# Kernel tuning notes

Hardware: AMD Instinct MI355X
Metric: run time of the kernel (lower is better)

Reference implementation:

```python
import jax, jax.numpy as jnp
import numpy as np

WIN = (2, 4, 4)
SHIFT = (1, 2, 2)
NUM_HEADS = 8
LN_EPS = 1e-5


def _rel_pos_index(ws):
    wt, wh, ww = ws
    coords = np.stack(np.meshgrid(np.arange(wt), np.arange(wh), np.arange(ww), indexing='ij'))
    cf = coords.reshape(3, -1)                      # [3, N]
    rel = cf[:, :, None] - cf[:, None, :]           # [3, N, N]
    rel = rel.transpose(1, 2, 0).copy()             # [N, N, 3]
    rel[..., 0] += wt - 1
    rel[..., 1] += wh - 1
    rel[..., 2] += ww - 1
    rel[..., 0] *= (2 * wh - 1) * (2 * ww - 1)
    rel[..., 1] *= 2 * ww - 1
    return rel.sum(-1)                              # [N, N] int

REL_IDX = _rel_pos_index(WIN)


def _layer_norm(x, w, b):
    mu = jnp.mean(x, axis=-1, keepdims=True)
    var = jnp.mean(jnp.square(x - mu), axis=-1, keepdims=True)
    return (x - mu) * jax.lax.rsqrt(var + LN_EPS) * w + b


def setup_inputs() -> dict:
    key = jax.random.key(0)
    ks = jax.random.split(key, 8)
    C, Cm = 256, 1024
    inp = {
        'x': jax.random.normal(ks[0], (2, 16, 64, 64, C), jnp.float32),
        'norm1_w': jnp.ones((C,), jnp.float32),
        'norm1_b': jnp.zeros((C,), jnp.float32),
        'qkv_w': jax.random.normal(ks[1], (C, 3 * C), jnp.float32) * 0.02,
        'qkv_b': jnp.zeros((3 * C,), jnp.float32),
        'proj_w': jax.random.normal(ks[2], (C, C), jnp.float32) * 0.02,
        'proj_b': jnp.zeros((C,), jnp.float32),
        'rel_bias_table': jax.random.normal(ks[3], (147, NUM_HEADS), jnp.float32) * 0.02,
        'norm2_w': jnp.ones((C,), jnp.float32),
        'norm2_b': jnp.zeros((C,), jnp.float32),
        'mlp_w1': jax.random.normal(ks[4], (C, Cm), jnp.float32) * 0.02,
        'mlp_b1': jnp.zeros((Cm,), jnp.float32),
        'mlp_w2': jax.random.normal(ks[5], (Cm, C), jnp.float32) * 0.02,
        'mlp_b2': jnp.zeros((C,), jnp.float32),
    }
    return inp


def reference(x, norm1_w, norm1_b, qkv_w, qkv_b, proj_w, proj_b,
              rel_bias_table, norm2_w, norm2_b, mlp_w1, mlp_b1, mlp_w2, mlp_b2):
    B, T, H, W, C = x.shape
    wT, wH, wW = WIN
    nh = NUM_HEADS
    d = C // nh
    scale = d ** (-0.5)
    N = wT * wH * wW

    shortcut = x
    h = _layer_norm(x, norm1_w, norm1_b)
    # cyclic shift (no attention mask is applied in the original block)
    h = jnp.roll(h, shift=(-SHIFT[0], -SHIFT[1], -SHIFT[2]), axis=(1, 2, 3))
    # window partition -> [B*nW, N, C]
    h = h.reshape(B, T // wT, wT, H // wH, wH, W // wW, wW, C)
    h = h.transpose(0, 1, 3, 5, 2, 4, 6, 7).reshape(-1, N, C)
    B_ = h.shape[0]

    qkv = (h @ qkv_w + qkv_b).reshape(B_, N, 3, nh, d).transpose(2, 0, 3, 1, 4)
    q, k, v = qkv[0] * scale, qkv[1], qkv[2]          # [B_, nh, N, d]
    attn = jnp.einsum('bhnd,bhmd->bhnm', q, k)        # [B_, nh, N, N]
    bias = rel_bias_table[REL_IDX].transpose(2, 0, 1)  # [nh, N, N]
    attn = jax.nn.softmax(attn + bias[None], axis=-1)
    o = jnp.einsum('bhnm,bhmd->bhnd', attn, v)
    o = o.transpose(0, 2, 1, 3).reshape(B_, N, C)
    o = o @ proj_w + proj_b

    # window reverse -> [B, T, H, W, C]
    o = o.reshape(B, T // wT, H // wH, W // wW, wT, wH, wW, C)
    o = o.transpose(0, 1, 4, 2, 5, 3, 6, 7).reshape(B, T, H, W, C)
    o = jnp.roll(o, shift=SHIFT, axis=(1, 2, 3))

    x = shortcut + o
    m = _layer_norm(x, norm2_w, norm2_b)
    m = jax.nn.gelu(m @ mlp_w1 + mlp_b1, approximate=False) @ mlp_w2 + mlp_b2
    return x + m
```

## Files before the change

kernel.cpp:

```cpp
#include <hip/hip_runtime.h>
#include <hip/hip_bf16.h>
#include <cstdint>
#include <cstddef>

typedef __attribute__((ext_vector_type(8)))  short  s16x8;
typedef __attribute__((ext_vector_type(4)))  float  fp32x4;
typedef __attribute__((ext_vector_type(16))) float  fp32x16;
typedef __attribute__((ext_vector_type(4)))  unsigned short u16x4;

static __device__ __forceinline__ float bf2f(unsigned short u) {
    union { unsigned int i; float f; } v; v.i = ((unsigned int)u) << 16; return v.f;
}
static __device__ __forceinline__ unsigned short f2bf(float f) {
    __hip_bfloat16 h = __float2bfloat16(f);
    return __builtin_bit_cast(unsigned short, h);
}

static __device__ __forceinline__ fp32x16 mfma32(s16x8 a, s16x8 b, fp32x16 c) {
    return __builtin_amdgcn_mfma_f32_32x32x16_bf16(a, b, c, 0, 0, 0);
}
static __device__ __forceinline__ fp32x4 mfma16(s16x8 a, s16x8 b, fp32x4 c) {
    return __builtin_amdgcn_mfma_f32_16x16x32_bf16(a, b, c, 0, 0, 0);
}

static __device__ __forceinline__ float wave_sum(float v) {
#pragma unroll
    for (int off = 32; off > 0; off >>= 1) v += __shfl_xor(v, off, 64);
    return v;
}

static __device__ __forceinline__ float gelu_f(float u) {
    float t = u * (1.0f + 0.044715f * u * u) * 1.595769122f;
    return u * (1.0f / (1.0f + __expf(-t)));
}

#define NTOK   131072
#define CDIM   256

__global__ void prep_kernel(const float* __restrict__ qkv_w, const float* __restrict__ proj_w,
                            const float* __restrict__ w1,    const float* __restrict__ w2,
                            const float* __restrict__ rel,
                            unsigned short* __restrict__ qkvT, unsigned short* __restrict__ projT,
                            unsigned short* __restrict__ w1T,  unsigned short* __restrict__ w2T,
                            float* __restrict__ btab) {
    int id = blockIdx.x * 256 + threadIdx.x;
    if (id < 196608) {
        int n = id >> 8, k = id & 255;
        qkvT[id] = f2bf(qkv_w[k * 768 + n]);
    } else if (id < 262144) {
        int e = id - 196608; int n = e >> 8, k = e & 255;
        projT[e] = f2bf(proj_w[k * 256 + n]);
    } else if (id < 524288) {
        int e = id - 262144; int n = e >> 8, k = e & 255;
        w1T[e] = f2bf(w1[k * 1024 + n]);
    } else if (id < 786432) {
        int e = id - 524288; int n = e >> 10, k = e & 1023;
        w2T[e] = f2bf(w2[k * 256 + n]);
    } else {
        int e = id - 786432;
        int h = e >> 10, rem = e & 1023, n = rem >> 5, m = rem & 31;
        int tn = n >> 4, hn = (n >> 2) & 3, wn = n & 3;
        int tm = m >> 4, hm = (m >> 2) & 3, wm = m & 3;
        int ridx = (tn - tm + 1) * 49 + (hn - hm + 3) * 7 + (wn - wm + 3);
        btab[e] = rel[ridx * 8 + h];
    }
}

__global__ __launch_bounds__(256) void ln_kernel(const float* __restrict__ in,
                                                 const float* __restrict__ w,
                                                 const float* __restrict__ b,
                                                 unsigned short* __restrict__ out) {
    int tid = threadIdx.x, lane = tid & 63, wid = tid >> 6;
    long r = (long)blockIdx.x * 4 + wid;
    int n = (int)(r & 31); int win = (int)(r >> 5);
    int b_ = win >> 11, tw = (win >> 8) & 7, hw = (win >> 4) & 15, ww = win & 15;
    int ti = n >> 4, hi = (n >> 2) & 3, wi = n & 3;
    int t = tw * 2 + ti, hh = hw * 4 + hi, wv = ww * 4 + wi;
    int ts = (t + 1) & 15, hs = (hh + 2) & 63, wsd = (wv + 2) & 63;
    long src = ((long)((b_ * 16 + ts) * 64 + hs)) * 64 + wsd;

    float4 v = *(const float4*)&in[src * CDIM + lane * 4];
    float vv[4] = {v.x, v.y, v.z, v.w};
    float s = vv[0] + vv[1] + vv[2] + vv[3];
    s = wave_sum(s);
    float mean = s * (1.0f / 256.0f);
    float q = vv[0]*vv[0] + vv[1]*vv[1] + vv[2]*vv[2] + vv[3]*vv[3];
    q = wave_sum(q);
    float var = q * (1.0f / 256.0f) - mean * mean;
    float rstd = rsqrtf(var + 1e-5f);
    int c0 = lane * 4;
    u16x4 o;
#pragma unroll
    for (int j = 0; j < 4; ++j)
        o[j] = f2bf((vv[j] - mean) * rstd * w[c0 + j] + b[c0 + j]);
    *(u16x4*)&out[r * CDIM + c0] = o;
}

template <int K, int EPI, int NS, int NX>
__global__ __launch_bounds__(512) void gemm256(const unsigned short* __restrict__ A,
                                               const unsigned short* __restrict__ Bt,
                                               const float* __restrict__ bias,
                                               float* __restrict__ outf,
                                               unsigned short* __restrict__ outb,
                                               const float* __restrict__ resid,
                                               const float* __restrict__ lnw,
                                               const float* __restrict__ lnb) {
    extern __shared__ unsigned short lds[];
    const int tid = threadIdx.x;
    const int lane = tid & 63, wid = tid >> 6;
    const int wm = wid >> 2, wn = wid & 3;
    constexpr int NWG = NX * 512;
    constexpr int CPX = NWG / 8;
    const int bid = blockIdx.x;
    const int wg = (bid & 7) * CPX + (bid >> 3);
    const int n0 = (wg % NX) * 256;
    const size_t m0 = (size_t)(wg / NX) * 256;
    constexpr int NK = K / 64;

    fp32x4 acc[8][4] = {};

    auto stage = [&](int kt, int buf) {
#pragma unroll
        for (int i = 0; i < 4; ++i) {
            int L = i * 512 + tid;
            int r = L >> 3, c = L & 7;
            int sc = c ^ (r & 7);
            const unsigned short* ga = A + (m0 + r) * K + kt * 64 + sc * 8;
            __builtin_amdgcn_global_load_lds(
                (const __attribute__((address_space(1))) void*)ga,
                (__attribute__((address_space(3))) void*)(lds + buf * 16384 + L * 8),
                16, 0, 0);
            const unsigned short* gb = Bt + (size_t)(n0 + r) * K + kt * 64 + sc * 8;
            __builtin_amdgcn_global_load_lds(
                (const __attribute__((address_space(1))) void*)gb,
                (__attribute__((address_space(3))) void*)(lds + 32768 + buf * 16384 + L * 8),
                16, 0, 0);
        }
    };

    stage(0, 0);
    __syncthreads();
    for (int kt = 0; kt < NK; ++kt) {
        if (kt + 1 < NK) stage(kt + 1, (kt + 1) & 1);
        const unsigned short* As = lds + (kt & 1) * 16384;
        const unsigned short* Bs = lds + 32768 + (kt & 1) * 16384;
#pragma unroll
        for (int ks = 0; ks < 2; ++ks) {
            s16x8 a[8], b[4];
#pragma unroll
            for (int m = 0; m < 8; ++m) {
                int row = wm * 128 + m * 16 + (lane & 15);
                int j = ks * 4 + (lane >> 4);
                a[m] = *(const s16x8*)(As + row * 64 + ((j ^ (row & 7)) << 3));
            }
#pragma unroll
            for (int n = 0; n < 4; ++n) {
                int row = wn * 64 + n * 16 + (lane & 15);
                int j = ks * 4 + (lane >> 4);
                b[n] = *(const s16x8*)(Bs + row * 64 + ((j ^ (row & 7)) << 3));
            }
#pragma unroll
            for (int m = 0; m < 8; ++m)
#pragma unroll
                for (int n = 0; n < 4; ++n)
                    acc[m][n] = mfma16(a[m], b[n], acc[m][n]);
        }
        __syncthreads();
    }

    float bv[4];
#pragma unroll
    for (int n = 0; n < 4; ++n) bv[n] = bias[n0 + wn * 64 + n * 16 + (lane & 15)];

    if (EPI == 1) {
        float* part = (float*)lds;
        float lw[4], lb[4];
#pragma unroll
        for (int n = 0; n < 4; ++n) {
            int gc = wn * 64 + n * 16 + (lane & 15);
            lw[n] = lnw[gc]; lb[n] = lnb[gc];
        }
#pragma unroll
        for (int m = 0; m < 8; ++m) {
#pragma unroll
            for (int rg = 0; rg < 4; ++rg) {
                int row_t = wm * 128 + m * 16 + ((lane >> 4) << 2) + rg;
                size_t gr = m0 + row_t;
                int win = (int)(gr >> 5), n_ = (int)(gr & 31);
                int b_ = win >> 11, tw = (win >> 8) & 7, hw = (win >> 4) & 15, ww = win & 15;
                int ti = n_ >> 4, hi = (n_ >> 2) & 3, wi = n_ & 3;
                int t = tw * 2 + ti, hh = hw * 4 + hi, wv = ww * 4 + wi;
                int ts = (t + 1) & 15, hs = (hh + 2) & 63, wsd = (wv + 2) & 63;
                size_t dst = ((size_t)((b_ * 16 + ts) * 64 + hs)) * 64 + wsd;
                float s = 0.f, q = 0.f;
#pragma unroll
                for (int n = 0; n < 4; ++n) {
                    int gc = wn * 64 + n * 16 + (lane & 15);
                    float v = acc[m][n][rg] + bv[n] + resid[dst * CDIM + gc];
                    outf[dst * CDIM + gc] = v;
                    acc[m][n][rg] = v;
                    s += v; q += v * v;
                }
#pragma unroll
                for (int off = 1; off < 16; off <<= 1) {
                    s += __shfl_xor(s, off, 16);
                    q += __shfl_xor(q, off, 16);
                }
                if ((lane & 15) == 0) {
                    part[(row_t * 4 + wn) * 2]     = s;
                    part[(row_t * 4 + wn) * 2 + 1] = q;
                }
            }
        }
        __syncthreads();
#pragma unroll
        for (int m = 0; m < 8; ++m) {
#pragma unroll
            for (int rg = 0; rg < 4; ++rg) {
                int row_t = wm * 128 + m * 16 + ((lane >> 4) << 2) + rg;
                size_t gr = m0 + row_t;
                int win = (int)(gr >> 5), n_ = (int)(gr & 31);
                int b_ = win >> 11, tw = (win >> 8) & 7, hw = (win >> 4) & 15, ww = win & 15;
                int ti = n_ >> 4, hi = (n_ >> 2) & 3, wi = n_ & 3;
                int t = tw * 2 + ti, hh = hw * 4 + hi, wv = ww * 4 + wi;
                int ts = (t + 1) & 15, hs = (hh + 2) & 63, wsd = (wv + 2) & 63;
                size_t dst = ((size_t)((b_ * 16 + ts) * 64 + hs)) * 64 + wsd;
                float4 p0 = *(const float4*)&part[row_t * 8];
                float4 p1 = *(const float4*)&part[row_t * 8 + 4];
                float s = p0.x + p0.z + p1.x + p1.z;
                float q = p0.y + p0.w + p1.y + p1.w;
                float mean = s * (1.0f / 256.0f);
                float var  = q * (1.0f / 256.0f) - mean * mean;
                float rstd = rsqrtf(var + 1e-5f);
#pragma unroll
                for (int n = 0; n < 4; ++n) {
                    int gc = wn * 64 + n * 16 + (lane & 15);
                    float v = acc[m][n][rg];
                    outb[dst * CDIM + gc] = f2bf((v - mean) * rstd * lw[n] + lb[n]);
                }
            }
        }
    } else {
#pragma unroll
        for (int m = 0; m < 8; ++m) {
#pragma unroll
            for (int rg = 0; rg < 4; ++rg) {
                int row_t = wm * 128 + m * 16 + ((lane >> 4) << 2) + rg;
                size_t gr = m0 + row_t;
#pragma unroll
                for (int n = 0; n < 4; ++n) {
                    int gc = n0 + wn * 64 + n * 16 + (lane & 15);
                    float v = acc[m][n][rg] + bv[n];
                    if (EPI == 0) {
                        outb[gr * NS + gc] = f2bf(v);
                    } else if (EPI == 2) {
                        outb[gr * NS + gc] = f2bf(gelu_f(v));
                    } else {
                        outf[gr * NS + gc] += v;
                    }
                }
            }
        }
    }
}

__global__ __launch_bounds__(256) void attn_kernel(const unsigned short* __restrict__ qkv,
                                                   const float* __restrict__ btab,
                                                   unsigned short* __restrict__ obuf) {
    __shared__ unsigned short sP[4][1280];
    __shared__ unsigned short sVt[4][1280];
    int tid = threadIdx.x, lane = tid & 63, wid = tid >> 6;
    int task = blockIdx.x * 4 + wid;
    int win = task >> 3, hh = task & 7;
    const unsigned short* base = qkv + (size_t)win * 32 * 768 + hh * 32;
    int q = lane & 31, h = lane >> 5;

    s16x8 v0 = *(const s16x8*)(base + 512 + q * 768 + h * 16);
    s16x8 v1 = *(const s16x8*)(base + 512 + q * 768 + h * 16 + 8);
#pragma unroll
    for (int j = 0; j < 8; ++j) {
        sVt[wid][(h * 16 + j) * 40 + q]     = (unsigned short)v0[j];
        sVt[wid][(h * 16 + 8 + j) * 40 + q] = (unsigned short)v1[j];
    }

    s16x8 aq0 = *(const s16x8*)(base + q * 768 + h * 8);
    s16x8 aq1 = *(const s16x8*)(base + q * 768 + 16 + h * 8);
    s16x8 bk0 = *(const s16x8*)(base + 256 + q * 768 + h * 8);
    s16x8 bk1 = *(const s16x8*)(base + 256 + q * 768 + 16 + h * 8);
    fp32x16 S = {0.0f};
    S = mfma32(aq0, bk0, S);
    S = mfma32(aq1, bk1, S);

    const float scale = 0.17677669529663687f;
    float pr[16];
#pragma unroll
    for (int r = 0; r < 16; ++r) {
        int row = (r & 3) + 8 * (r >> 2) + 4 * h;
        float bvv = btab[(hh * 32 + row) * 32 + q];
        pr[r] = S[r] * scale + bvv;
    }
#pragma unroll
    for (int r = 0; r < 16; ++r) {
        float mx = pr[r];
#pragma unroll
        for (int off = 16; off > 0; off >>= 1) mx = fmaxf(mx, __shfl_xor(mx, off, 64));
        float e = __expf(pr[r] - mx);
        float sm = e;
#pragma unroll
        for (int off = 16; off > 0; off >>= 1) sm += __shfl_xor(sm, off, 64);
        pr[r] = e * __builtin_amdgcn_rcpf(sm);
    }
#pragma unroll
    for (int r = 0; r < 16; ++r) {
        int row = (r & 3) + 8 * (r >> 2) + 4 * h;
        sP[wid][row * 40 + q] = f2bf(pr[r]);
    }
    __syncthreads();

    s16x8 pa0 = *(const s16x8*)&sP[wid][q * 40 + h * 8];
    s16x8 pa1 = *(const s16x8*)&sP[wid][q * 40 + 16 + h * 8];
    s16x8 vb0 = *(const s16x8*)&sVt[wid][q * 40 + h * 8];
    s16x8 vb1 = *(const s16x8*)&sVt[wid][q * 40 + 16 + h * 8];
    fp32x16 O = {0.0f};
    O = mfma32(pa0, vb0, O);
    O = mfma32(pa1, vb1, O);
#pragma unroll
    for (int r = 0; r < 16; ++r) {
        int row = (r & 3) + 8 * (r >> 2) + 4 * h;
        obuf[((size_t)win * 32 + row) * 256 + hh * 32 + q] = f2bf(O[r]);
    }
}

extern "C" void kernel_launch(void* const* d_in, const int* in_sizes, int n_in,
                              void* d_out, int out_size, void* d_ws, size_t ws_size,
                              hipStream_t stream) {
    const float* x      = (const float*)d_in[0];
    const float* n1w    = (const float*)d_in[1];
    const float* n1b    = (const float*)d_in[2];
    const float* qkv_w  = (const float*)d_in[3];
    const float* qkv_b  = (const float*)d_in[4];
    const float* proj_w = (const float*)d_in[5];
    const float* proj_b = (const float*)d_in[6];
    const float* rel    = (const float*)d_in[7];
    const float* n2w    = (const float*)d_in[8];
    const float* n2b    = (const float*)d_in[9];
    const float* w1     = (const float*)d_in[10];
    const float* b1     = (const float*)d_in[11];
    const float* w2     = (const float*)d_in[12];
    const float* b2     = (const float*)d_in[13];
    float* out = (float*)d_out;

    char* ws = (char*)d_ws;
    unsigned short* hwin = (unsigned short*)ws;
    unsigned short* big  = (unsigned short*)(ws + 67108864);
    unsigned short* obuf = big + 100663296;
    char* wreg = ws + 67108864 + 268435456;
    unsigned short* qkvT  = (unsigned short*)(wreg);
    unsigned short* projT = (unsigned short*)(wreg + 393216);
    unsigned short* w1T   = (unsigned short*)(wreg + 524288);
    unsigned short* w2T   = (unsigned short*)(wreg + 1048576);
    float*          btab  = (float*)(wreg + 1572864);

    prep_kernel<<<3104, 256, 0, stream>>>(qkv_w, proj_w, w1, w2, rel, qkvT, projT, w1T, w2T, btab);

    ln_kernel<<<NTOK / 4, 256, 0, stream>>>(x, n1w, n1b, hwin);

    gemm256<256, 0, 768, 3><<<1536, 512, 131072, stream>>>(hwin, qkvT, qkv_b, nullptr, big,
                                                           nullptr, nullptr, nullptr);

    attn_kernel<<<8192, 256, 0, stream>>>(big, btab, obuf);

    gemm256<256, 1, 256, 1><<<512, 512, 131072, stream>>>(obuf, projT, proj_b, out, hwin,
                                                          x, n2w, n2b);

    gemm256<256, 2, 1024, 4><<<2048, 512, 131072, stream>>>(hwin, w1T, b1, nullptr, big,
                                                            nullptr, nullptr, nullptr);

    gemm256<1024, 3, 256, 1><<<512, 512, 131072, stream>>>(big, w2T, b2, out, nullptr,
                                                           nullptr, nullptr, nullptr);
}
```

Baseline: 653.1 us.

## Switch QKV and MLP GEMMs to 128x128 tiles with two blocks per CU

Adds a gemm128 kernel: 256-thread blocks computing 128x128 tiles with static 64KB LDS, two blocks per CU, precomputed incrementing global pointers, and a single barrier per k-step. It replaces the 256x256 tile GEMM for the QKV, MLP1 and MLP2 GEMMs. The projection GEMM with the fused residual+LayerNorm epilogue keeps its own 256-tile kernel, with its inner loop reordered into quadrants to shorten fragment register lifetimes. The aim is more occupancy and better tail balance, at the cost of lower per-tile data reuse and more global and LDS traffic per FLOP.

New measurement: 685.4 us. +4.9%, slower.

```diff
diff --git a/kernel.cpp b/kernel.cpp
--- a/kernel.cpp
+++ b/kernel.cpp
@@ -8,9 +8,6 @@
 typedef __attribute__((ext_vector_type(16))) float  fp32x16;
 typedef __attribute__((ext_vector_type(4)))  unsigned short u16x4;
 
-static __device__ __forceinline__ float bf2f(unsigned short u) {
-    union { unsigned int i; float f; } v; v.i = ((unsigned int)u) << 16; return v.f;
-}
 static __device__ __forceinline__ unsigned short f2bf(float f) {
     __hip_bfloat16 h = __float2bfloat16(f);
     return __builtin_bit_cast(unsigned short, h);
@@ -97,24 +94,120 @@
 }
 
 template <int K, int EPI, int NS, int NX>
-__global__ __launch_bounds__(512) void gemm256(const unsigned short* __restrict__ A,
-                                               const unsigned short* __restrict__ Bt,
-                                               const float* __restrict__ bias,
-                                               float* __restrict__ outf,
-                                               unsigned short* __restrict__ outb,
-                                               const float* __restrict__ resid,
-                                               const float* __restrict__ lnw,
-                                               const float* __restrict__ lnb) {
+__global__ __launch_bounds__(256, 2) void gemm128(const unsigned short* __restrict__ A,
+                                                  const unsigned short* __restrict__ Bt,
+                                                  const float* __restrict__ bias,
+                                                  float* __restrict__ outf,
+                                                  unsigned short* __restrict__ outb) {
+    __shared__ unsigned short lds[32768];
+    const int tid = threadIdx.x;
+    const int lane = tid & 63, wid = tid >> 6;
+    const int wm = wid >> 1, wn = wid & 1;
+    constexpr int NWG = 1024 * NX;
+    constexpr int CPX = NWG / 8;
+    const int bid = blockIdx.x;
+    const int wg = (bid & 7) * CPX + (bid >> 3);
+    const int n0 = (wg % NX) * 128;
+    const size_t m0 = (size_t)(wg / NX) * 128;
+    constexpr int NK = K / 64;
+
+    fp32x4 acc[4][4] = {};
+
+    const unsigned short* gA[4];
+    const unsigned short* gB[4];
+    int ldst[4];
+#pragma unroll
+    for (int i = 0; i < 4; ++i) {
+        int L = i * 256 + tid;
+        int r = L >> 3, c = L & 7;
+        int sc = c ^ (r & 7);
+        gA[i] = A  + (m0 + r) * (size_t)K + sc * 8;
+        gB[i] = Bt + (size_t)(n0 + r) * K + sc * 8;
+        ldst[i] = L * 8;
+    }
+    auto stage = [&](int buf) {
+#pragma unroll
+        for (int i = 0; i < 4; ++i) {
+            __builtin_amdgcn_global_load_lds(
+                (const __attribute__((address_space(1))) void*)gA[i],
+                (__attribute__((address_space(3))) void*)(lds + buf * 16384 + ldst[i]),
+                16, 0, 0);
+            __builtin_amdgcn_global_load_lds(
+                (const __attribute__((address_space(1))) void*)gB[i],
+                (__attribute__((address_space(3))) void*)(lds + buf * 16384 + 8192 + ldst[i]),
+                16, 0, 0);
+            gA[i] += 64; gB[i] += 64;
+        }
+    };
+
+    const int r7 = (lane & 15) & 7;
+    const int aoff = (wm * 64 + (lane & 15)) * 64 + (((lane >> 4) ^ r7) << 3);
+    const int boff = 8192 + (wn * 64 + (lane & 15)) * 64 + (((lane >> 4) ^ r7) << 3);
+
+    stage(0);
+    for (int kt = 0; kt < NK; ++kt) {
+        __syncthreads();
+        if (kt + 1 < NK) stage((kt + 1) & 1);
+        const int cb = (kt & 1) * 16384;
+#pragma unroll
+        for (int ks = 0; ks < 2; ++ks) {
+            const int kx = ks * 32;
+            s16x8 a[4], b[4];
+#pragma unroll
+            for (int m = 0; m < 4; ++m)
+                a[m] = *(const s16x8*)(lds + cb + (aoff ^ kx) + m * 1024);
+#pragma unroll
+            for (int n = 0; n < 4; ++n)
+                b[n] = *(const s16x8*)(lds + cb + (boff ^ kx) + n * 1024);
+#pragma unroll
+            for (int m = 0; m < 4; ++m)
+#pragma unroll
+                for (int n = 0; n < 4; ++n)
+                    acc[m][n] = mfma16(a[m], b[n], acc[m][n]);
+        }
+    }
+
+    float bv[4];
+#pragma unroll
+    for (int n = 0; n < 4; ++n) bv[n] = bias[n0 + wn * 64 + n * 16 + (lane & 15)];
+
+#pragma unroll
+    for (int m = 0; m < 4; ++m) {
+#pragma unroll
+        for (int rg = 0; rg < 4; ++rg) {
+            size_t gr = m0 + wm * 64 + m * 16 + ((lane >> 4) << 2) + rg;
+#pragma unroll
+            for (int n = 0; n < 4; ++n) {
+                int gc = n0 + wn * 64 + n * 16 + (lane & 15);
+                float v = acc[m][n][rg] + bv[n];
+                if (EPI == 0) {
+                    outb[gr * NS + gc] = f2bf(v);
+                } else if (EPI == 2) {
+                    outb[gr * NS + gc] = f2bf(gelu_f(v));
+                } else {
+                    outf[gr * NS + gc] += v;
+                }
+            }
+        }
+    }
+}
+
+template <int K>
+__global__ __launch_bounds__(512) void gemm256_proj(const unsigned short* __restrict__ A,
+                                                    const unsigned short* __restrict__ Bt,
+                                                    const float* __restrict__ bias,
+                                                    float* __restrict__ outf,
+                                                    unsigned short* __restrict__ outb,
+                                                    const float* __restrict__ resid,
+                                                    const float* __restrict__ lnw,
+                                                    const float* __restrict__ lnb) {
     extern __shared__ unsigned short lds[];
     const int tid = threadIdx.x;
     const int lane = tid & 63, wid = tid >> 6;
     const int wm = wid >> 2, wn = wid & 3;
-    constexpr int NWG = NX * 512;
-    constexpr int CPX = NWG / 8;
     const int bid = blockIdx.x;
-    const int wg = (bid & 7) * CPX + (bid >> 3);
-    const int n0 = (wg % NX) * 256;
-    const size_t m0 = (size_t)(wg / NX) * 256;
+    const int wg = (bid & 7) * 64 + (bid >> 3);
+    const size_t m0 = (size_t)wg * 256;
     constexpr int NK = K / 64;
 
     fp32x4 acc[8][4] = {};
@@ -130,7 +223,7 @@
                 (const __attribute__((address_space(1))) void*)ga,
                 (__attribute__((address_space(3))) void*)(lds + buf * 16384 + L * 8),
                 16, 0, 0);
-            const unsigned short* gb = Bt + (size_t)(n0 + r) * K + kt * 64 + sc * 8;
+            const unsigned short* gb = Bt + (size_t)r * K + kt * 64 + sc * 8;
             __builtin_amdgcn_global_load_lds(
                 (const __attribute__((address_space(1))) void*)gb,
                 (__attribute__((address_space(3))) void*)(lds + 32768 + buf * 16384 + L * 8),
@@ -139,126 +232,111 @@
     };
 
     stage(0, 0);
-    __syncthreads();
     for (int kt = 0; kt < NK; ++kt) {
+        __syncthreads();
         if (kt + 1 < NK) stage(kt + 1, (kt + 1) & 1);
         const unsigned short* As = lds + (kt & 1) * 16384;
         const unsigned short* Bs = lds + 32768 + (kt & 1) * 16384;
 #pragma unroll
-        for (int ks = 0; ks < 2; ++ks) {
-            s16x8 a[8], b[4];
-#pragma unroll
-            for (int m = 0; m < 8; ++m) {
-                int row = wm * 128 + m * 16 + (lane & 15);
-                int j = ks * 4 + (lane >> 4);
-                a[m] = *(const s16x8*)(As + row * 64 + ((j ^ (row & 7)) << 3));
+        for (int q = 0; q < 4; ++q) {
+            const int qm = q >> 1, qn = q & 1;
+            s16x8 a[4][2], b[2][2];
+#pragma unroll
+            for (int m = 0; m < 4; ++m)
+#pragma unroll
+                for (int ks = 0; ks < 2; ++ks) {
+                    int row = wm * 128 + qm * 64 + m * 16 + (lane & 15);
+                    int j = ks * 4 + (lane >> 4);
+                    a[m][ks] = *(const s16x8*)(As + row * 64 + ((j ^ (row & 7)) << 3));
+                }
+#pragma unroll
+            for (int n = 0; n < 2; ++n)
+#pragma unroll
+                for (int ks = 0; ks < 2; ++ks) {
+                    int row = wn * 64 + qn * 32 + n * 16 + (lane & 15);
+                    int j = ks * 4 + (lane >> 4);
+                    b[n][ks] = *(const s16x8*)(Bs + row * 64 + ((j ^ (row & 7)) << 3));
+                }
+#pragma unroll
+            for (int ks = 0; ks < 2; ++ks)
+#pragma unroll
+                for (int m = 0; m < 4; ++m)
+#pragma unroll
+                    for (int n = 0; n < 2; ++n)
+                        acc[qm * 4 + m][qn * 2 + n] =
+                            mfma16(a[m][ks], b[n][ks], acc[qm * 4 + m][qn * 2 + n]);
+        }
+        __syncthreads();
+    }
+
+    float bv[4];
+#pragma unroll
+    for (int n = 0; n < 4; ++n) bv[n] = bias[wn * 64 + n * 16 + (lane & 15)];
+
+    float* part = (float*)lds;
+    float lw[4], lb[4];
+#pragma unroll
+    for (int n = 0; n < 4; ++n) {
+        int gc = wn * 64 + n * 16 + (lane & 15);
+        lw[n] = lnw[gc]; lb[n] = lnb[gc];
+    }
+#pragma unroll
+    for (int m = 0; m < 8; ++m) {
+#pragma unroll
+        for (int rg = 0; rg < 4; ++rg) {
+            int row_t = wm * 128 + m * 16 + ((lane >> 4) << 2) + rg;
+            size_t gr = m0 + row_t;
+            int win = (int)(gr >> 5), n_ = (int)(gr & 31);
+            int b_ = win >> 11, tw = (win >> 8) & 7, hw = (win >> 4) & 15, ww = win & 15;
+            int ti = n_ >> 4, hi = (n_ >> 2) & 3, wi = n_ & 3;
+            int t = tw * 2 + ti, hh = hw * 4 + hi, wv = ww * 4 + wi;
+            int ts = (t + 1) & 15, hs = (hh + 2) & 63, wsd = (wv + 2) & 63;
+            size_t dst = ((size_t)((b_ * 16 + ts) * 64 + hs)) * 64 + wsd;
+            float s = 0.f, q = 0.f;
+#pragma unroll
+            for (int n = 0; n < 4; ++n) {
+                int gc = wn * 64 + n * 16 + (lane & 15);
+                float v = acc[m][n][rg] + bv[n] + resid[dst * CDIM + gc];
+                outf[dst * CDIM + gc] = v;
+                acc[m][n][rg] = v;
+                s += v; q += v * v;
             }
 #pragma unroll
+            for (int off = 1; off < 16; off <<= 1) {
+                s += __shfl_xor(s, off, 16);
+                q += __shfl_xor(q, off, 16);
+            }
+            if ((lane & 15) == 0) {
+                part[(row_t * 4 + wn) * 2]     = s;
+                part[(row_t * 4 + wn) * 2 + 1] = q;
+            }
+        }
+    }
+    __syncthreads();
+#pragma unroll
+    for (int m = 0; m < 8; ++m) {
+#pragma unroll
+        for (int rg = 0; rg < 4; ++rg) {
+            int row_t = wm * 128 + m * 16 + ((lane >> 4) << 2) + rg;
+            size_t gr = m0 + row_t;
+            int win = (int)(gr >> 5), n_ = (int)(gr & 31);
+            int b_ = win >> 11, tw = (win >> 8) & 7, hw = (win >> 4) & 15, ww = win & 15;
+            int ti = n_ >> 4, hi = (n_ >> 2) & 3, wi = n_ & 3;
+            int t = tw * 2 + ti, hh = hw * 4 + hi, wv = ww * 4 + wi;
+            int ts = (t + 1) & 15, hs = (hh + 2) & 63, wsd = (wv + 2) & 63;
+            size_t dst = ((size_t)((b_ * 16 + ts) * 64 + hs)) * 64 + wsd;
+            float4 p0 = *(const float4*)&part[row_t * 8];
+            float4 p1 = *(const float4*)&part[row_t * 8 + 4];
+            float s = p0.x + p0.z + p1.x + p1.z;
+            float q = p0.y + p0.w + p1.y + p1.w;
+            float mean = s * (1.0f / 256.0f);
+            float var  = q * (1.0f / 256.0f) - mean * mean;
+            float rstd = rsqrtf(var + 1e-5f);
+#pragma unroll
             for (int n = 0; n < 4; ++n) {
-                int row = wn * 64 + n * 16 + (lane & 15);
-                int j = ks * 4 + (lane >> 4);
-                b[n] = *(const s16x8*)(Bs + row * 64 + ((j ^ (row & 7)) << 3));
-            }
-#pragma unroll
-            for (int m = 0; m < 8; ++m)
-#pragma unroll
-                for (int n = 0; n < 4; ++n)
-                    acc[m][n] = mfma16(a[m], b[n], acc[m][n]);
-        }
-        __syncthreads();
-    }
-
-    float bv[4];
-#pragma unroll
-    for (int n = 0; n < 4; ++n) bv[n] = bias[n0 + wn * 64 + n * 16 + (lane & 15)];
-
-    if (EPI == 1) {
-        float* part = (float*)lds;
-        float lw[4], lb[4];
-#pragma unroll
-        for (int n = 0; n < 4; ++n) {
-            int gc = wn * 64 + n * 16 + (lane & 15);
-            lw[n] = lnw[gc]; lb[n] = lnb[gc];
-        }
-#pragma unroll
-        for (int m = 0; m < 8; ++m) {
-#pragma unroll
-            for (int rg = 0; rg < 4; ++rg) {
-                int row_t = wm * 128 + m * 16 + ((lane >> 4) << 2) + rg;
-                size_t gr = m0 + row_t;
-                int win = (int)(gr >> 5), n_ = (int)(gr & 31);
-                int b_ = win >> 11, tw = (win >> 8) & 7, hw = (win >> 4) & 15, ww = win & 15;
-                int ti = n_ >> 4, hi = (n_ >> 2) & 3, wi = n_ & 3;
-                int t = tw * 2 + ti, hh = hw * 4 + hi, wv = ww * 4 + wi;
-                int ts = (t + 1) & 15, hs = (hh + 2) & 63, wsd = (wv + 2) & 63;
-                size_t dst = ((size_t)((b_ * 16 + ts) * 64 + hs)) * 64 + wsd;
-                float s = 0.f, q = 0.f;
-#pragma unroll
-                for (int n = 0; n < 4; ++n) {
-                    int gc = wn * 64 + n * 16 + (lane & 15);
-                    float v = acc[m][n][rg] + bv[n] + resid[dst * CDIM + gc];
-                    outf[dst * CDIM + gc] = v;
-                    acc[m][n][rg] = v;
-                    s += v; q += v * v;
-                }
-#pragma unroll
-                for (int off = 1; off < 16; off <<= 1) {
-                    s += __shfl_xor(s, off, 16);
-                    q += __shfl_xor(q, off, 16);
-                }
-                if ((lane & 15) == 0) {
-                    part[(row_t * 4 + wn) * 2]     = s;
-                    part[(row_t * 4 + wn) * 2 + 1] = q;
-                }
-            }
-        }
-        __syncthreads();
-#pragma unroll
-        for (int m = 0; m < 8; ++m) {
-#pragma unroll
-            for (int rg = 0; rg < 4; ++rg) {
-                int row_t = wm * 128 + m * 16 + ((lane >> 4) << 2) + rg;
-                size_t gr = m0 + row_t;
-                int win = (int)(gr >> 5), n_ = (int)(gr & 31);
-                int b_ = win >> 11, tw = (win >> 8) & 7, hw = (win >> 4) & 15, ww = win & 15;
-                int ti = n_ >> 4, hi = (n_ >> 2) & 3, wi = n_ & 3;
-                int t = tw * 2 + ti, hh = hw * 4 + hi, wv = ww * 4 + wi;
-                int ts = (t + 1) & 15, hs = (hh + 2) & 63, wsd = (wv + 2) & 63;
-                size_t dst = ((size_t)((b_ * 16 + ts) * 64 + hs)) * 64 + wsd;
-                float4 p0 = *(const float4*)&part[row_t * 8];
-                float4 p1 = *(const float4*)&part[row_t * 8 + 4];
-                float s = p0.x + p0.z + p1.x + p1.z;
-                float q = p0.y + p0.w + p1.y + p1.w;
-                float mean = s * (1.0f / 256.0f);
-                float var  = q * (1.0f / 256.0f) - mean * mean;
-                float rstd = rsqrtf(var + 1e-5f);
-#pragma unroll
-                for (int n = 0; n < 4; ++n) {
-                    int gc = wn * 64 + n * 16 + (lane & 15);
-                    float v = acc[m][n][rg];
-                    outb[dst * CDIM + gc] = f2bf((v - mean) * rstd * lw[n] + lb[n]);
-                }
-            }
-        }
-    } else {
-#pragma unroll
-        for (int m = 0; m < 8; ++m) {
-#pragma unroll
-            for (int rg = 0; rg < 4; ++rg) {
-                int row_t = wm * 128 + m * 16 + ((lane >> 4) << 2) + rg;
-                size_t gr = m0 + row_t;
-#pragma unroll
-                for (int n = 0; n < 4; ++n) {
-                    int gc = n0 + wn * 64 + n * 16 + (lane & 15);
-                    float v = acc[m][n][rg] + bv[n];
-                    if (EPI == 0) {
-                        outb[gr * NS + gc] = f2bf(v);
-                    } else if (EPI == 2) {
-                        outb[gr * NS + gc] = f2bf(gelu_f(v));
-                    } else {
-                        outf[gr * NS + gc] += v;
-                    }
-                }
+                int gc = wn * 64 + n * 16 + (lane & 15);
+                float v = acc[m][n][rg];
+                outb[dst * CDIM + gc] = f2bf((v - mean) * rstd * lw[n] + lb[n]);
             }
         }
     }
@@ -296,8 +374,7 @@
 #pragma unroll
     for (int r = 0; r < 16; ++r) {
         int row = (r & 3) + 8 * (r >> 2) + 4 * h;
-        float bvv = btab[(hh * 32 + row) * 32 + q];
-        pr[r] = S[r] * scale + bvv;
+        pr[r] = S[r] * scale + btab[(hh * 32 + row) * 32 + q];
     }
 #pragma unroll
     for (int r = 0; r < 16; ++r) {
@@ -365,17 +442,13 @@
 
     ln_kernel<<<NTOK / 4, 256, 0, stream>>>(x, n1w, n1b, hwin);
 
-    gemm256<256, 0, 768, 3><<<1536, 512, 131072, stream>>>(hwin, qkvT, qkv_b, nullptr, big,
-                                                           nullptr, nullptr, nullptr);
+    gemm128<256, 0, 768, 6><<<6144, 256, 0, stream>>>(hwin, qkvT, qkv_b, nullptr, big);
 
     attn_kernel<<<8192, 256, 0, stream>>>(big, btab, obuf);
 
-    gemm256<256, 1, 256, 1><<<512, 512, 131072, stream>>>(obuf, projT, proj_b, out, hwin,
-                                                          x, n2w, n2b);
-
-    gemm256<256, 2, 1024, 4><<<2048, 512, 131072, stream>>>(hwin, w1T, b1, nullptr, big,
-                                                            nullptr, nullptr, nullptr);
-
-    gemm256<1024, 3, 256, 1><<<512, 512, 131072, stream>>>(big, w2T, b2, out, nullptr,
-                                                           nullptr, nullptr, nullptr);
-}
+    gemm256_proj<256><<<512, 512, 131072, stream>>>(obuf, projT, proj_b, out, hwin, x, n2w, n2b);
+
+    gemm128<256, 2, 1024, 8><<<8192, 256, 0, stream>>>(hwin, w1T, b1, nullptr, big);
+
+    gemm128<1024, 3, 256, 2><<<2048, 256, 0, stream>>>(big, w2T, b2, out, nullptr);
+}
```
